# Kernel optimization log

Measured on AMD Instinct MI355X. Metric: run time of the kernel, lower is better.

Reference implementation:

```python
import jax, jax.numpy as jnp
import numpy as np

WEIGHT = 0.1
TEMPERATURE = 0.07
EPS_NORM = 1e-12   # F.normalize eps
EPS_DEN = 1e-6     # denominator eps in pos_mask.sum()


def setup_inputs() -> dict:
    key = jax.random.key(0)
    k1, k2 = jax.random.split(key)
    features = jax.random.normal(k1, (4, 1000, 2048), dtype=jnp.float32)
    target = jax.random.randint(k2, (4, 1000), 0, 16, dtype=jnp.int64)
    return {"features": features, "target": target}


def _per_sample_loss(f, t):
    # f: [N, C], t: [N]
    N = f.shape[0]
    # F.normalize(dim=1)
    norm = jnp.maximum(jnp.linalg.norm(f, axis=1, keepdims=True), EPS_NORM)
    f = f / norm
    # [N, N] cosine similarities scaled by temperature
    sim = jnp.matmul(f, f.T) / TEMPERATURE
    eye = jnp.eye(N, dtype=f.dtype)
    pos = (t[:, None] == t[None, :]).astype(f.dtype) * (1.0 - eye)
    neg = 1.0 - pos - eye
    pos_sim = sim * pos
    # -log(exp(pos_sim) / (exp(pos_sim) + sum_j exp(sim)*neg))  summed over ALL entries
    denom = jnp.exp(pos_sim) + jnp.sum(jnp.exp(sim) * neg, axis=1, keepdims=True)
    loss_mat = jnp.log(denom) - pos_sim
    pos_sum = pos.sum()
    return loss_mat.sum() / (pos_sum + EPS_DEN), pos_sum


def reference(features, target):
    # features: [B, N, C] (already 3-D: no subsampling / interpolation paths fire)
    losses, pos_sums = jax.vmap(_per_sample_loss)(features, target)
    valid = pos_sums > 0
    num_pairs = valid.sum().astype(features.dtype)
    total = jnp.where(valid, losses, 0.0).sum()
    return jnp.where(num_pairs > 0, WEIGHT * total / num_pairs,
                     jnp.asarray(WEIGHT * 0.1, dtype=features.dtype))
```

## Files before the change

### kernel.cpp

```cpp
#include <hip/hip_runtime.h>
#include <math.h>

#define BB 4
#define NN 1000
#define NP 1024
#define CC 2048
#define TINV (1.0f / 0.07f)

#define FNORM_BYTES ((size_t)BB * NP * CC * 2)
#define SIM_BYTES   ((size_t)BB * NP * NP * 4)
#define RL_BYTES    ((size_t)BB * NP * 4)

typedef __bf16 bf16x8 __attribute__((ext_vector_type(8)));
typedef float  f32x4  __attribute__((ext_vector_type(4)));

__device__ __forceinline__ void load_lds16(const void* g, void* l) {
    __builtin_amdgcn_global_load_lds(
        (const __attribute__((address_space(1))) unsigned int*)g,
        (__attribute__((address_space(3))) unsigned int*)l, 16, 0, 0);
}

__device__ __forceinline__ float blk_sum(float v, volatile float* lds) {
    int lane = threadIdx.x & 63;
    int wid  = threadIdx.x >> 6;
#pragma unroll
    for (int off = 32; off; off >>= 1) v += __shfl_down(v, off);
    __syncthreads();
    if (lane == 0) lds[wid] = v;
    __syncthreads();
    return lds[0] + lds[1] + lds[2] + lds[3];
}

__device__ __forceinline__ float wave_sum(float v) {
#pragma unroll
    for (int off = 32; off; off >>= 1) v += __shfl_down(v, off);
    return __shfl(v, 0);
}

__global__ __launch_bounds__(256) void norm_bf16_kernel(const float* __restrict__ f,
                                                        __bf16* __restrict__ out) {
    __shared__ float lds[4];
    __shared__ float scale_s;
    const int blk = blockIdx.x;
    const int b = blk >> 10, r = blk & (NP - 1);
    __bf16* dst = out + ((size_t)b * NP + r) * CC;
    const int tid = threadIdx.x;

    if (r >= NN) {
        ((uint4*)dst)[tid] = make_uint4(0u, 0u, 0u, 0u);
        return;
    }
    const float* src = f + ((size_t)b * NN + r) * CC;

    float ss = 0.f;
#pragma unroll
    for (int h = 0; h < 2; ++h) {
        float4 v = ((const float4*)src)[tid + h * 256];
        ss += v.x * v.x + v.y * v.y + v.z * v.z + v.w * v.w;
    }
    float tot = blk_sum(ss, lds);
    if (tid == 0) scale_s = 1.0f / fmaxf(sqrtf(tot), 1e-12f);
    __syncthreads();
    const float sc = scale_s;

    float4 v0 = ((const float4*)src)[tid * 2];
    float4 v1 = ((const float4*)src)[tid * 2 + 1];
    bf16x8 o;
    o[0] = (__bf16)(v0.x * sc); o[1] = (__bf16)(v0.y * sc);
    o[2] = (__bf16)(v0.z * sc); o[3] = (__bf16)(v0.w * sc);
    o[4] = (__bf16)(v1.x * sc); o[5] = (__bf16)(v1.y * sc);
    o[6] = (__bf16)(v1.z * sc); o[7] = (__bf16)(v1.w * sc);
    *(bf16x8*)(dst + tid * 8) = o;
}

__global__ __launch_bounds__(512) void simgemm_mfma(const __bf16* __restrict__ fn,
                                                    float* __restrict__ sim) {
    __shared__ __bf16 As[128 * 32];
    __shared__ __bf16 Bs[128 * 32];

    const int b  = blockIdx.z;
    const int tI = blockIdx.y * 128;
    const int tJ = blockIdx.x * 128;
    const __bf16* base = fn + (size_t)b * NP * CC;
    float* S = sim + (size_t)b * NP * NP;

    const int tid  = threadIdx.x;
    const int wid  = tid >> 6;
    const int lane = tid & 63;
    const int wm   = wid >> 2;
    const int wn   = wid & 3;
    const int q    = lane >> 4;
    const int ln   = lane & 15;

    const int srow  = wid * 16 + (lane >> 2);
    const int selem = (lane & 3) * 8;
    const __bf16* gA = base + (size_t)(tI + srow) * CC + selem;
    const __bf16* gB = base + (size_t)(tJ + srow) * CC + selem;
    __bf16* lA = As + wid * 512;
    __bf16* lB = Bs + wid * 512;

    f32x4 acc[4][2] = {};

    for (int k0 = 0; k0 < CC; k0 += 32) {
        load_lds16(gA + k0, lA);
        load_lds16(gB + k0, lB);
        __syncthreads();

        bf16x8 af[4], bf[2];
#pragma unroll
        for (int mt = 0; mt < 4; ++mt)
            af[mt] = *(const bf16x8*)&As[(wm * 64 + mt * 16 + ln) * 32 + q * 8];
#pragma unroll
        for (int nt = 0; nt < 2; ++nt)
            bf[nt] = *(const bf16x8*)&Bs[(wn * 32 + nt * 16 + ln) * 32 + q * 8];
#pragma unroll
        for (int mt = 0; mt < 4; ++mt)
#pragma unroll
            for (int nt = 0; nt < 2; ++nt)
                acc[mt][nt] = __builtin_amdgcn_mfma_f32_16x16x32_bf16(
                    af[mt], bf[nt], acc[mt][nt], 0, 0, 0);
        __syncthreads();
    }

#pragma unroll
    for (int mt = 0; mt < 4; ++mt) {
#pragma unroll
        for (int nt = 0; nt < 2; ++nt) {
            const int col = tJ + wn * 32 + nt * 16 + ln;
#pragma unroll
            for (int r = 0; r < 4; ++r) {
                const int row = tI + wm * 64 + mt * 16 + q * 4 + r;
                S[(size_t)row * NP + col] = acc[mt][nt][r] * TINV;
            }
        }
    }
}

__global__ __launch_bounds__(256) void rowloss_kernel(const float* __restrict__ sim,
                                                      const int* __restrict__ tgt,
                                                      float* __restrict__ rloss,
                                                      float* __restrict__ rpos) {
    __shared__ int ts[NN];
    const int b = blockIdx.y;
    const int wid = threadIdx.x >> 6, lane = threadIdx.x & 63;
    const int* t = tgt + (size_t)b * NN;
    for (int j = threadIdx.x; j < NN; j += 256) ts[j] = t[j];
    __syncthreads();

    const int i = blockIdx.x * 4 + wid;
    const float* row = sim + ((size_t)b * NP + i) * NP;
    const int ti = ts[i];

    float sneg = 0.f, pcnt = 0.f;
    for (int g = lane; g < NN / 4; g += 64) {
        float4 v = ((const float4*)row)[g];
        int4 tj = *(const int4*)&ts[g * 4];
        const int j = g * 4;
        if (j + 0 != i) { if (tj.x == ti) pcnt += 1.f; else sneg += __expf(v.x); }
        if (j + 1 != i) { if (tj.y == ti) pcnt += 1.f; else sneg += __expf(v.y); }
        if (j + 2 != i) { if (tj.z == ti) pcnt += 1.f; else sneg += __expf(v.z); }
        if (j + 3 != i) { if (tj.w == ti) pcnt += 1.f; else sneg += __expf(v.w); }
    }
    const float Sv = wave_sum(sneg);
    const float p  = wave_sum(pcnt);

    float term = 0.f;
    for (int g = lane; g < NN / 4; g += 64) {
        float4 v = ((const float4*)row)[g];
        int4 tj = *(const int4*)&ts[g * 4];
        const int j = g * 4;
        if (j + 0 != i && tj.x == ti) term += __logf(__expf(v.x) + Sv) - v.x;
        if (j + 1 != i && tj.y == ti) term += __logf(__expf(v.y) + Sv) - v.y;
        if (j + 2 != i && tj.z == ti) term += __logf(__expf(v.z) + Sv) - v.z;
        if (j + 3 != i && tj.w == ti) term += __logf(__expf(v.w) + Sv) - v.w;
    }
    const float tt = wave_sum(term);
    if (lane == 0) {
        rloss[b * NP + i] = tt + ((float)NN - p) * __logf(1.f + Sv);
        rpos [b * NP + i] = p;
    }
}

__global__ __launch_bounds__(256) void final_kernel(const float* __restrict__ rloss,
                                                    const float* __restrict__ rpos,
                                                    float* __restrict__ out) {
    __shared__ float lds[4];
    float total = 0.f, np = 0.f;
    for (int b = 0; b < BB; ++b) {
        float l = 0.f, p = 0.f;
        for (int i = threadIdx.x; i < NN; i += 256) {
            l += rloss[b * NP + i];
            p += rpos [b * NP + i];
        }
        float ls = blk_sum(l, lds);
        float ps = blk_sum(p, lds);
        if (ps > 0.f) { total += ls / (ps + 1e-6f); np += 1.f; }
    }
    if (threadIdx.x == 0)
        out[0] = (np > 0.f) ? 0.1f * total / np : 0.1f * 0.1f;
}

extern "C" void kernel_launch(void* const* d_in, const int* in_sizes, int n_in,
                              void* d_out, int out_size, void* d_ws, size_t ws_size,
                              hipStream_t stream) {
    const float* feat = (const float*)d_in[0];
    const int*   tgt  = (const int*)d_in[1];
    __bf16* fnorm = (__bf16*)d_ws;
    float*  sim   = (float*)((char*)d_ws + FNORM_BYTES);
    float*  rloss = (float*)((char*)d_ws + FNORM_BYTES + SIM_BYTES);
    float*  rpos  = (float*)((char*)d_ws + FNORM_BYTES + SIM_BYTES + RL_BYTES);

    norm_bf16_kernel<<<dim3(BB * NP), 256, 0, stream>>>(feat, fnorm);
    simgemm_mfma<<<dim3(NP / 128, NP / 128, BB), 512, 0, stream>>>(fnorm, sim);
    rowloss_kernel<<<dim3(NN / 4, BB), 256, 0, stream>>>(sim, tgt, rloss, rpos);
    final_kernel<<<1, 256, 0, stream>>>(rloss, rpos, (float*)d_out);
}
```

Measured before the change: 130.9 us.

## Fuse contrastive loss partials into GEMM epilogue instead of materialising sim matrix

The GEMM epilogue now reads the targets itself. For each row within each 128-column tile it accumulates the sum of exp over negative pairs and stores the positive similarities in fixed LDS slots. A small follow-up kernel combines the per-tile partials into per-row losses. This removes the write and re-read of the full B×N×N float similarity matrix. In exchange it adds LDS atomics and cross-lane shuffles to the epilogue. Positives per row per tile are capped at 32 slots, so any extra positives are silently dropped; that is safe only while labels stay spread across enough classes.

```diff
diff --git a/kernel.cpp b/kernel.cpp
--- a/kernel.cpp
+++ b/kernel.cpp
@@ -6,9 +6,12 @@
 #define NP 1024
 #define CC 2048
 #define TINV (1.0f / 0.07f)
+#define CTS 8
+#define PSLOTS 32
 
 #define FNORM_BYTES ((size_t)BB * NP * CC * 2)
-#define SIM_BYTES   ((size_t)BB * NP * NP * 4)
+#define PN_BYTES    ((size_t)BB * CTS * NP * 4)
+#define PL_BYTES    ((size_t)BB * CTS * NP * PSLOTS * 4)
 #define RL_BYTES    ((size_t)BB * NP * 4)
 
 typedef __bf16 bf16x8 __attribute__((ext_vector_type(8)));
@@ -29,12 +32,6 @@
     if (lane == 0) lds[wid] = v;
     __syncthreads();
     return lds[0] + lds[1] + lds[2] + lds[3];
-}
-
-__device__ __forceinline__ float wave_sum(float v) {
-#pragma unroll
-    for (int off = 32; off; off >>= 1) v += __shfl_down(v, off);
-    return __shfl(v, 0);
 }
 
 __global__ __launch_bounds__(256) void norm_bf16_kernel(const float* __restrict__ f,
@@ -73,16 +70,22 @@
     *(bf16x8*)(dst + tid * 8) = o;
 }
 
-__global__ __launch_bounds__(512) void simgemm_mfma(const __bf16* __restrict__ fn,
-                                                    float* __restrict__ sim) {
+__global__ __launch_bounds__(512) void fused_gemm_loss(const __bf16* __restrict__ fn,
+                                                       const int* __restrict__ tgt,
+                                                       float* __restrict__ Pn,
+                                                       int* __restrict__ Cn,
+                                                       float* __restrict__ PL) {
     __shared__ __bf16 As[128 * 32];
     __shared__ __bf16 Bs[128 * 32];
+    __shared__ int   ts[NP];
+    __shared__ float Pl[128][4];
+    __shared__ float posl[128][PSLOTS];
+    __shared__ int   pcl[128];
 
     const int b  = blockIdx.z;
     const int tI = blockIdx.y * 128;
     const int tJ = blockIdx.x * 128;
     const __bf16* base = fn + (size_t)b * NP * CC;
-    float* S = sim + (size_t)b * NP * NP;
 
     const int tid  = threadIdx.x;
     const int wid  = tid >> 6;
@@ -92,6 +95,10 @@
     const int q    = lane >> 4;
     const int ln   = lane & 15;
 
+    const int* t = tgt + (size_t)b * NN;
+    for (int j = tid; j < NP; j += 512) ts[j] = (j < NN) ? t[j] : -1;
+    if (tid < 128) pcl[tid] = 0;
+
     const int srow  = wid * 16 + (lane >> 2);
     const int selem = (lane & 3) * 8;
     const __bf16* gA = base + (size_t)(tI + srow) * CC + selem;
@@ -122,63 +129,94 @@
         __syncthreads();
     }
 
+    float sneg[16];
+#pragma unroll
+    for (int k = 0; k < 16; ++k) sneg[k] = 0.f;
+
 #pragma unroll
     for (int mt = 0; mt < 4; ++mt) {
+        int gi4[4], tr4[4];
+#pragma unroll
+        for (int r = 0; r < 4; ++r) {
+            const int rloc = wm * 64 + mt * 16 + q * 4 + r;
+            gi4[r] = tI + rloc;
+            tr4[r] = ts[tI + rloc];
+        }
 #pragma unroll
         for (int nt = 0; nt < 2; ++nt) {
-            const int col = tJ + wn * 32 + nt * 16 + ln;
+            const int cloc = wn * 32 + nt * 16 + ln;
+            const int gj   = tJ + cloc;
+            const int tc   = ts[gj];
+            const bool jvalid = (gj < NN);
 #pragma unroll
             for (int r = 0; r < 4; ++r) {
-                const int row = tI + wm * 64 + mt * 16 + q * 4 + r;
-                S[(size_t)row * NP + col] = acc[mt][nt][r] * TINV;
+                const float s = acc[mt][nt][r] * TINV;
+                if (jvalid && gj != gi4[r]) {
+                    if (tc == tr4[r]) {
+                        const int rloc = wm * 64 + mt * 16 + q * 4 + r;
+                        int slot = atomicAdd(&pcl[rloc], 1);
+                        if (slot < PSLOTS) posl[rloc][slot] = s;
+                    } else {
+                        sneg[mt * 4 + r] += __expf(s);
+                    }
+                }
             }
         }
     }
-}
-
-__global__ __launch_bounds__(256) void rowloss_kernel(const float* __restrict__ sim,
-                                                      const int* __restrict__ tgt,
-                                                      float* __restrict__ rloss,
-                                                      float* __restrict__ rpos) {
-    __shared__ int ts[NN];
+#pragma unroll
+    for (int m = 1; m < 16; m <<= 1)
+#pragma unroll
+        for (int k = 0; k < 16; ++k) sneg[k] += __shfl_xor(sneg[k], m);
+    if (ln == 0) {
+#pragma unroll
+        for (int mt = 0; mt < 4; ++mt)
+#pragma unroll
+            for (int r = 0; r < 4; ++r)
+                Pl[wm * 64 + mt * 16 + q * 4 + r][wn] = sneg[mt * 4 + r];
+    }
+    __syncthreads();
+
+    const size_t tileo = ((size_t)(b * CTS + blockIdx.x)) * NP + tI;
+    if (tid < 128) {
+        Pn[tileo + tid] = Pl[tid][0] + Pl[tid][1] + Pl[tid][2] + Pl[tid][3];
+        Cn[tileo + tid] = min(pcl[tid], PSLOTS);
+    }
+    {
+        const float4* src = (const float4*)&posl[0][0];
+        float4* dst = (float4*)&PL[tileo * PSLOTS];
+        dst[tid]       = src[tid];
+        dst[tid + 512] = src[tid + 512];
+    }
+}
+
+__global__ __launch_bounds__(256) void rowloss2_kernel(const float* __restrict__ Pn,
+                                                       const int* __restrict__ Cn,
+                                                       const float* __restrict__ PL,
+                                                       float* __restrict__ rloss,
+                                                       float* __restrict__ rpos) {
     const int b = blockIdx.y;
-    const int wid = threadIdx.x >> 6, lane = threadIdx.x & 63;
-    const int* t = tgt + (size_t)b * NN;
-    for (int j = threadIdx.x; j < NN; j += 256) ts[j] = t[j];
-    __syncthreads();
-
-    const int i = blockIdx.x * 4 + wid;
-    const float* row = sim + ((size_t)b * NP + i) * NP;
-    const int ti = ts[i];
-
-    float sneg = 0.f, pcnt = 0.f;
-    for (int g = lane; g < NN / 4; g += 64) {
-        float4 v = ((const float4*)row)[g];
-        int4 tj = *(const int4*)&ts[g * 4];
-        const int j = g * 4;
-        if (j + 0 != i) { if (tj.x == ti) pcnt += 1.f; else sneg += __expf(v.x); }
-        if (j + 1 != i) { if (tj.y == ti) pcnt += 1.f; else sneg += __expf(v.y); }
-        if (j + 2 != i) { if (tj.z == ti) pcnt += 1.f; else sneg += __expf(v.z); }
-        if (j + 3 != i) { if (tj.w == ti) pcnt += 1.f; else sneg += __expf(v.w); }
-    }
-    const float Sv = wave_sum(sneg);
-    const float p  = wave_sum(pcnt);
-
-    float term = 0.f;
-    for (int g = lane; g < NN / 4; g += 64) {
-        float4 v = ((const float4*)row)[g];
-        int4 tj = *(const int4*)&ts[g * 4];
-        const int j = g * 4;
-        if (j + 0 != i && tj.x == ti) term += __logf(__expf(v.x) + Sv) - v.x;
-        if (j + 1 != i && tj.y == ti) term += __logf(__expf(v.y) + Sv) - v.y;
-        if (j + 2 != i && tj.z == ti) term += __logf(__expf(v.z) + Sv) - v.z;
-        if (j + 3 != i && tj.w == ti) term += __logf(__expf(v.w) + Sv) - v.w;
-    }
-    const float tt = wave_sum(term);
-    if (lane == 0) {
-        rloss[b * NP + i] = tt + ((float)NN - p) * __logf(1.f + Sv);
-        rpos [b * NP + i] = p;
-    }
+    const int i = blockIdx.x * 256 + threadIdx.x;
+    if (i >= NN) return;
+
+    float S = 0.f;
+#pragma unroll
+    for (int ct = 0; ct < CTS; ++ct)
+        S += Pn[(size_t)(b * CTS + ct) * NP + i];
+
+    float term = 0.f, p = 0.f;
+#pragma unroll
+    for (int ct = 0; ct < CTS; ++ct) {
+        const size_t o = (size_t)(b * CTS + ct) * NP + i;
+        const int c = Cn[o];
+        p += (float)c;
+        const float* pl = &PL[o * PSLOTS];
+        for (int k = 0; k < c; ++k) {
+            const float s = pl[k];
+            term += __logf(__expf(s) + S) - s;
+        }
+    }
+    rloss[b * NP + i] = term + ((float)NN - p) * __logf(1.f + S);
+    rpos [b * NP + i] = p;
 }
 
 __global__ __launch_bounds__(256) void final_kernel(const float* __restrict__ rloss,
@@ -205,13 +243,16 @@
                               hipStream_t stream) {
     const float* feat = (const float*)d_in[0];
     const int*   tgt  = (const int*)d_in[1];
-    __bf16* fnorm = (__bf16*)d_ws;
-    float*  sim   = (float*)((char*)d_ws + FNORM_BYTES);
-    float*  rloss = (float*)((char*)d_ws + FNORM_BYTES + SIM_BYTES);
-    float*  rpos  = (float*)((char*)d_ws + FNORM_BYTES + SIM_BYTES + RL_BYTES);
+    char* ws = (char*)d_ws;
+    __bf16* fnorm = (__bf16*)ws;                               ws += FNORM_BYTES;
+    float*  Pn    = (float*)ws;                                ws += PN_BYTES;
+    int*    Cn    = (int*)ws;                                  ws += PN_BYTES;
+    float*  PL    = (float*)ws;                                ws += PL_BYTES;
+    float*  rloss = (float*)ws;                                ws += RL_BYTES;
+    float*  rpos  = (float*)ws;
 
     norm_bf16_kernel<<<dim3(BB * NP), 256, 0, stream>>>(feat, fnorm);
-    simgemm_mfma<<<dim3(NP / 128, NP / 128, BB), 512, 0, stream>>>(fnorm, sim);
-    rowloss_kernel<<<dim3(NN / 4, BB), 256, 0, stream>>>(sim, tgt, rloss, rpos);
+    fused_gemm_loss<<<dim3(CTS, NP / 128, BB), 512, 0, stream>>>(fnorm, tgt, Pn, Cn, PL);
+    rowloss2_kernel<<<dim3(NP / 256, BB), 256, 0, stream>>>(Pn, Cn, PL, rloss, rpos);
     final_kernel<<<1, 256, 0, stream>>>(rloss, rpos, (float*)d_out);
 }
```

Result: slower. 147.6 us (+12.8%).
